# Optimization experiments

Measured on AMD Instinct MI355X. Metric: run time of the kernel, lower is better.

The kernel has to match this reference:

```python
import jax, jax.numpy as jnp
import numpy as np

B, S, V, H, L, NH, DH, F = 1, 512, 30522, 768, 12, 12, 64, 3072
N, E, GH, NC = 50000, 800000, 128, 3


def setup_inputs() -> dict:
    key = jax.random.key(0)
    ks = iter(jax.random.split(key, 48))
    def nrm(shape, s=0.02):
        return jax.random.normal(next(ks), shape, jnp.float32) * s
    inp = {
        "input_ids": jax.random.randint(next(ks), (B, S), 0, V, dtype=jnp.int32),
        "attention_mask": jnp.ones((B, S), jnp.int32),
        "token_type_ids": jnp.zeros((B, S), jnp.int32),
        "premise_edge_index": jax.random.randint(next(ks), (2, E), 0, N, dtype=jnp.int32),
        "hypothesis_edge_index": jax.random.randint(next(ks), (2, E), 0, N, dtype=jnp.int32),
        "premise_node_features": nrm((N, H), 1.0),
        "hypothesis_node_features": nrm((N, H), 1.0),
        "word_emb": nrm((V, H)), "pos_emb": nrm((S, H)), "type_emb": nrm((2, H)),
        "emb_ln_s": jnp.ones((H,)), "emb_ln_b": jnp.zeros((H,)),
        "Wq": nrm((L, H, H)), "bq": jnp.zeros((L, H)),
        "Wk": nrm((L, H, H)), "bk": jnp.zeros((L, H)),
        "Wv": nrm((L, H, H)), "bv": jnp.zeros((L, H)),
        "Wo": nrm((L, H, H)), "bo": jnp.zeros((L, H)),
        "ln1_s": jnp.ones((L, H)), "ln1_b": jnp.zeros((L, H)),
        "W1": nrm((L, H, F)), "b1": jnp.zeros((L, F)),
        "W2": nrm((L, F, H)), "b2": jnp.zeros((L, H)),
        "ln2_s": jnp.ones((L, H)), "ln2_b": jnp.zeros((L, H)),
        "gcn_W1": nrm((H, GH), 0.05), "gcn_b1": jnp.zeros((GH,)),
        "gcn_W2": nrm((GH, GH), 0.05), "gcn_b2": jnp.zeros((GH,)),
        "comb_W": nrm((2 * (H + GH), H)), "comb_b": jnp.zeros((H,)),
        "cls_W": nrm((H, NC)), "cls_b": jnp.zeros((NC,)),
    }
    return inp


def _ln(x, s, b, eps=1e-12):
    m = jnp.mean(x, -1, keepdims=True)
    v = jnp.mean(jnp.square(x - m), -1, keepdims=True)
    return (x - m) * jax.lax.rsqrt(v + eps) * s + b


def _gcn(x, edge_index, W1, b1, W2, b2):
    # PyG GCNConv: add self-loops, symmetric D^-1/2 A D^-1/2 normalization,
    # linear transform first, then scatter-add messages at destination.
    n = x.shape[0]
    loops = jnp.arange(n, dtype=edge_index.dtype)
    src = jnp.concatenate([edge_index[0], loops])
    dst = jnp.concatenate([edge_index[1], loops])
    deg = jax.ops.segment_sum(jnp.ones(src.shape[0], jnp.float32), dst, num_segments=n)
    dinv = jnp.where(deg > 0, jax.lax.rsqrt(jnp.maximum(deg, 1e-12)), 0.0)
    norm = (dinv[src] * dinv[dst])[:, None]
    def conv(h, W, b):
        hw = h @ W
        return jax.ops.segment_sum(hw[src] * norm, dst, num_segments=n) + b
    h = jax.nn.relu(conv(x, W1, b1))
    h = conv(h, W2, b2)
    # global_mean_pool with batch=None -> single graph mean, shape [1, GH]
    return jnp.mean(h, axis=0, keepdims=True)


def _bert(input_ids, attention_mask, token_type_ids, word_emb, pos_emb, type_emb, emb_ln_s, emb_ln_b, layer_params):
    s = input_ids.shape[1]
    h = word_emb[input_ids] + pos_emb[None, :s] + type_emb[token_type_ids]
    h = _ln(h, emb_ln_s, emb_ln_b)
    bias = (1.0 - attention_mask.astype(jnp.float32))[:, None, None, :] * -1e4
    def step(h, p):
        wq, bq, wk, bk, wv, bv, wo, bo, l1s, l1b, w1, b1_, w2, b2_, l2s, l2b = p
        b_, s_, _ = h.shape
        q = (h @ wq + bq).reshape(b_, s_, NH, DH)
        k = (h @ wk + bk).reshape(b_, s_, NH, DH)
        v = (h @ wv + bv).reshape(b_, s_, NH, DH)
        scores = jnp.einsum('bqhd,bkhd->bhqk', q, k) / np.float32(np.sqrt(DH)) + bias
        ctx = jnp.einsum('bhqk,bkhd->bqhd', jax.nn.softmax(scores, -1), v).reshape(b_, s_, H)
        h1 = _ln(h + ctx @ wo + bo, l1s, l1b)
        f = jax.nn.gelu(h1 @ w1 + b1_, approximate=False) @ w2 + b2_
        return _ln(h1 + f, l2s, l2b), None
    h, _ = jax.lax.scan(step, h, layer_params)
    return h[:, 0, :]  # CLS pooling, [B, H]


def reference(input_ids, attention_mask, token_type_ids, premise_edge_index, premise_node_features, hypothesis_edge_index, hypothesis_node_features, word_emb, pos_emb, type_emb, emb_ln_s, emb_ln_b, Wq, bq, Wk, bk, Wv, bv, Wo, bo, ln1_s, ln1_b, W1, b1, W2, b2, ln2_s, ln2_b, gcn_W1, gcn_b1, gcn_W2, gcn_b2, comb_W, comb_b, cls_W, cls_b):
    lp = (Wq, bq, Wk, bk, Wv, bv, Wo, bo, ln1_s, ln1_b, W1, b1, W2, b2, ln2_s, ln2_b)
    cls = _bert(input_ids, attention_mask, token_type_ids, word_emb, pos_emb, type_emb, emb_ln_s, emb_ln_b, lp)
    gp = _gcn(premise_node_features, premise_edge_index, gcn_W1, gcn_b1, gcn_W2, gcn_b2)
    gh = _gcn(hypothesis_node_features, hypothesis_edge_index, gcn_W1, gcn_b1, gcn_W2, gcn_b2)
    cp = jnp.concatenate([cls, gp], -1)
    ch = jnp.concatenate([cls, gh], -1)
    fc = jnp.concatenate([cp, ch], -1)  # [1, 2*(H+GH)]
    feat = jax.nn.relu(fc @ comb_W + comb_b)  # dropout is identity at eval
    return feat @ cls_W + cls_b
```

## Files before the change

### kernel.cpp

```cpp
#include <hip/hip_runtime.h>
#include <math.h>

constexpr int kS = 512, kH = 768, kNH = 12, kDH = 64, kF = 3072, kL = 12;
constexpr int kN = 50000, kE = 800000, kGH = 128;

#define CDIV(a,b) (((a)+(b)-1)/(b))

struct Ptr3 { const float* p[3]; };

typedef __attribute__((ext_vector_type(8))) short bf16x8;
typedef __attribute__((ext_vector_type(4))) float f32x4;

__device__ __forceinline__ unsigned short bf16_rne(float f) {
    unsigned int u = __float_as_uint(f);
    u += 0x7fffu + ((u >> 16) & 1u);
    return (unsigned short)(u >> 16);
}
__device__ __forceinline__ float bf16_f32(unsigned short h) {
    return __uint_as_float(((unsigned int)h) << 16);
}
__device__ __forceinline__ void split2(float f, short& hi, short& lo) {
    unsigned short h = bf16_rne(f);
    hi = (short)h;
    lo = (short)bf16_rne(f - bf16_f32(h));
// ... 54 lines not shown
        short hi, lo; split2(f, hi, lo);
        th[rr][c] = hi; tl[rr][c] = lo;
    }
    __syncthreads();
    #pragma unroll
    for (int p = 0; p < 4; p++) {
        int rr = p * 8 + r;
        Th[moff + (long)(n0 + rr) * K + k0 + c] = th[c][rr];
        Tl[moff + (long)(n0 + rr) * K + k0 + c] = tl[c][rr];
    }
}

__global__ void vtrans_kernel(const short* __restrict__ vh, const short* __restrict__ vl,
                              short* __restrict__ vth, short* __restrict__ vtl) {
    __shared__ short th[32][33], tl[32][33];
    int s0 = blockIdx.x * 32;
    int h = blockIdx.y >> 1, d0 = (blockIdx.y & 1) * 32;
    int c = threadIdx.x & 31, r = threadIdx.x >> 5;
    #pragma unroll
    for (int p = 0; p < 4; p++) {
        int rr = p * 8 + r;
        th[rr][c] = vh[(long)(s0 + rr) * kH + h * kDH + d0 + c];
        tl[rr][c] = vl[(long)(s0 + rr) * kH + h * kDH + d0 + c];
    }
    __syncthreads();
    #pragma unroll
    for (int p = 0; p < 4; p++) {
        int rr = p * 8 + r;
        vth[((long)h * kDH + d0 + rr) * kS + s0 + c] = th[c][rr];
        vtl[((long)h * kDH + d0 + rr) * kS + s0 + c] = tl[c][rr];
    }
}

__global__ __launch_bounds__(256, 4) void gemm_pre_kernel(
    const short* __restrict__ Ah, const short* __restrict__ Al,
    const short* __restrict__ Bth, const short* __restrict__ Btl, long wstride,
    float* __restrict__ part, int M, int Nn, int K, int S)
{
    __shared__ short As[128 * LDR], Bs[128 * LDR];
    int w = blockIdx.z / S, s = blockIdx.z % S;
    const short* Bh_ = Bth + (long)w * wstride;
    const short* Bl_ = Btl + (long)w * wstride;
    int Kc = K / S;
    int kbeg = s * Kc;
    int m0 = blockIdx.y * 128, n0 = blockIdx.x * 128;
    int tid = threadIdx.x;
    int sr = tid >> 1, sh16 = (tid & 1) * 16;
    const short* Agh = Ah + (long)(m0 + sr) * K + kbeg + sh16;
    const short* Agl = Al + (long)(m0 + sr) * K + kbeg + sh16;
    const short* Bgh = Bh_ + (long)(n0 + sr) * K + kbeg + sh16;
    const short* Bgl = Bl_ + (long)(n0 + sr) * K + kbeg + sh16;
    int lofs = sr * LDR + sh16;
    int wid = tid >> 6, lane = tid & 63;
    int wm = (wid >> 1) * 64, wn = (wid & 1) * 64;
    int fr = lane & 15, ko = (lane >> 4) * 8;
    f32x4 acc[4][4];
    #pragma unroll
    for (int i = 0; i < 4; i++)
        #pragma unroll
        for (int j = 0; j < 4; j++) acc[i][j] = (f32x4){0.f, 0.f, 0.f, 0.f};
    int nst = Kc / 32;
    for (int st = 0; st < nst; ++st) {
        int go = st * 32;
        *(bf16x8*)&As[lofs]      = *(const bf16x8*)(Agh + go);
        *(bf16x8*)&As[lofs + 8]  = *(const bf16x8*)(Agh + go + 8);
        *(bf16x8*)&As[lofs + 32] = *(const bf16x8*)(Agl + go);
        *(bf16x8*)&As[lofs + 40] = *(const bf16x8*)(Agl + go + 8);
        *(bf16x8*)&Bs[lofs]      = *(const bf16x8*)(Bgh + go);
        *(bf16x8*)&Bs[lofs + 8]  = *(const bf16x8*)(Bgh + go + 8);
        *(bf16x8*)&Bs[lofs + 32] = *(const bf16x8*)(Bgl + go);
        *(bf16x8*)&Bs[lofs + 40] = *(const bf16x8*)(Bgl + go + 8);
        __syncthreads();
        bf16x8 bh[4], bl[4];
        #pragma unroll
        for (int j = 0; j < 4; j++) {
            int c = (wn + j * 16 + fr) * LDR + ko;
            bh[j] = *(const bf16x8*)&Bs[c];
            bl[j] = *(const bf16x8*)&Bs[c + 32];
        }
        #pragma unroll
        for (int i = 0; i < 4; i++) {
            int r = (wm + i * 16 + fr) * LDR + ko;
            bf16x8 ah = *(const bf16x8*)&As[r];
            bf16x8 al = *(const bf16x8*)&As[r + 32];
            #pragma unroll
            for (int j = 0; j < 4; j++) {
                acc[i][j] = __builtin_amdgcn_mfma_f32_16x16x32_bf16(ah, bh[j], acc[i][j], 0, 0, 0);
                acc[i][j] = __builtin_amdgcn_mfma_f32_16x16x32_bf16(ah, bl[j], acc[i][j], 0, 0, 0);
                acc[i][j] = __builtin_amdgcn_mfma_f32_16x16x32_bf16(al, bh[j], acc[i][j], 0, 0, 0);
            }
        }
        __syncthreads();
    }
    long MN = (long)M * Nn;
    float* Pp = part + (long)(w * S + s) * MN;
    int cr = (lane >> 4) * 4;
    #pragma unroll
    for (int i = 0; i < 4; i++) {
        #pragma unroll
        for (int r = 0; r < 4; r++) {
            int gm = m0 + wm + i * 16 + cr + r;
            float* rowp = &Pp[(long)gm * Nn + n0 + wn + fr];
            #pragma unroll
            for (int j = 0; j < 4; j++) rowp[j * 16] = acc[i][j][r];
        }
    }
}

__global__ void splitk_epi_qkv_kernel(const float* __restrict__ part, Ptr3 bias,
                                      short* __restrict__ qh, short* __restrict__ ql,
                                      short* __restrict__ kh, short* __restrict__ kl,
                                      short* __restrict__ vh, short* __restrict__ vl,
                                      int S) {
    const long MN = (long)kS * kH;
    int w = blockIdx.y;
    long i = ((long)blockIdx.x * blockDim.x + threadIdx.x) * 4;
    if (i >= MN) return;
    const float* P = part + (long)w * S * MN + i;
    float4 a = *(const float4*)P;
    for (int s2 = 1; s2 < S; ++s2) {
        float4 b2 = *(const float4*)(P + (long)s2 * MN);
        a.x += b2.x; a.y += b2.y; a.z += b2.z; a.w += b2.w;
    }
    const float* bw = bias.p[w];
    int n = (int)(i % kH);
    a.x += bw[n]; a.y += bw[n + 1]; a.z += bw[n + 2]; a.w += bw[n + 3];
    short* oh = (w == 0) ? qh : (w == 1) ? kh : vh;
    short* ol = (w == 0) ? ql : (w == 1) ? kl : vl;
    short h0, l0, h1, l1, h2, l2, h3, l3;
    split2(a.x, h0, l0); split2(a.y, h1, l1); split2(a.z, h2, l2); split2(a.w, h3, l3);
    *(short4*)&oh[i] = make_short4(h0, h1, h2, h3);
    *(short4*)&ol[i] = make_short4(l0, l1, l2, l3);
}

__global__ void splitk_epi_sh_kernel(const float* __restrict__ part, const float* __restrict__ bias,
                                     short* __restrict__ oh, short* __restrict__ ol,
                                     long MN, int Nn, int S, int act) {
    long i = ((long)blockIdx.x * blockDim.x + threadIdx.x) * 4;
    if (i >= MN) return;
// ... 24 lines not shown
                                      const float* __restrict__ b, float* __restrict__ out,
                                      short* __restrict__ oh, short* __restrict__ ol, int S) {
    int row = blockIdx.x; int tid = threadIdx.x;
    __shared__ float red[256];
    const long MN = (long)kS * kH;
    float vals[3]; float sum = 0.f;
    #pragma unroll
    for (int r = 0; r < 3; r++) {
        int j = tid + r * 256;
        const float* P = part + (long)row * kH + j;
        float x = res[(long)row * kH + j] + bias[j];
        for (int s2 = 0; s2 < S; ++s2) x += P[(long)s2 * MN];
        vals[r] = x; sum += x;
    }
    red[tid] = sum; __syncthreads();
    for (int off = 128; off > 0; off >>= 1) { if (tid < off) red[tid] += red[tid + off]; __syncthreads(); }
    float mean = red[0] / kH; __syncthreads();
    float vs = 0.f;
    #pragma unroll
    for (int r = 0; r < 3; r++) { float d = vals[r] - mean; vs += d * d; }
    red[tid] = vs; __syncthreads();
    for (int off = 128; off > 0; off >>= 1) { if (tid < off) red[tid] += red[tid + off]; __syncthreads(); }
    float rstd = rsqrtf(red[0] / kH + 1e-12f);
    #pragma unroll
    for (int r = 0; r < 3; r++) {
        int j = tid + r * 256;
        float o = (vals[r] - mean) * rstd * g[j] + b[j];
        out[(long)row * kH + j] = o;
        short hi, lo; split2(o, hi, lo);
        oh[(long)row * kH + j] = hi; ol[(long)row * kH + j] = lo;
    }
}

__global__ __launch_bounds__(256, 4) void attn_scores_pre_kernel(
    const short* __restrict__ qh, const short* __restrict__ ql,
    const short* __restrict__ kh, const short* __restrict__ kl,
    const float* __restrict__ mb, float* __restrict__ scores)
{
    __shared__ short As[128 * LDR], Bs[128 * LDR];
    int h = blockIdx.z;
    int q0 = blockIdx.y * 128, k0 = blockIdx.x * 128;
    int tid = threadIdx.x;
    int sr = tid >> 1, sh16 = (tid & 1) * 16;
    const short* Agh = qh + (long)(q0 + sr) * kH + h * kDH + sh16;
    const short* Agl = ql + (long)(q0 + sr) * kH + h * kDH + sh16;
    const short* Bgh = kh + (long)(k0 + sr) * kH + h * kDH + sh16;
    const short* Bgl = kl + (long)(k0 + sr) * kH + h * kDH + sh16;
    int lofs = sr * LDR + sh16;
    int wid = tid >> 6, lane = tid & 63;
    int wm = (wid >> 1) * 64, wn = (wid & 1) * 64;
    int fr = lane & 15, ko = (lane >> 4) * 8;
    f32x4 acc[4][4];
    #pragma unroll
    for (int i = 0; i < 4; i++)
        #pragma unroll
        for (int j = 0; j < 4; j++) acc[i][j] = (f32x4){0.f, 0.f, 0.f, 0.f};
    #pragma unroll
    for (int st = 0; st < 2; ++st) {
        int go = st * 32;
        *(bf16x8*)&As[lofs]      = *(const bf16x8*)(Agh + go);
        *(bf16x8*)&As[lofs + 8]  = *(const bf16x8*)(Agh + go + 8);
        *(bf16x8*)&As[lofs + 32] = *(const bf16x8*)(Agl + go);
        *(bf16x8*)&As[lofs + 40] = *(const bf16x8*)(Agl + go + 8);
        *(bf16x8*)&Bs[lofs]      = *(const bf16x8*)(Bgh + go);
        *(bf16x8*)&Bs[lofs + 8]  = *(const bf16x8*)(Bgh + go + 8);
        *(bf16x8*)&Bs[lofs + 32] = *(const bf16x8*)(Bgl + go);
        *(bf16x8*)&Bs[lofs + 40] = *(const bf16x8*)(Bgl + go + 8);
        __syncthreads();
        bf16x8 bh[4], bl[4];
        #pragma unroll
        for (int j = 0; j < 4; j++) {
            int c = (wn + j * 16 + fr) * LDR + ko;
            bh[j] = *(const bf16x8*)&Bs[c];
            bl[j] = *(const bf16x8*)&Bs[c + 32];
        }
        #pragma unroll
        for (int i = 0; i < 4; i++) {
            int r = (wm + i * 16 + fr) * LDR + ko;
            bf16x8 ah = *(const bf16x8*)&As[r];
            bf16x8 al = *(const bf16x8*)&As[r + 32];
            #pragma unroll
            for (int j = 0; j < 4; j++) {
                acc[i][j] = __builtin_amdgcn_mfma_f32_16x16x32_bf16(ah, bh[j], acc[i][j], 0, 0, 0);
                acc[i][j] = __builtin_amdgcn_mfma_f32_16x16x32_bf16(ah, bl[j], acc[i][j], 0, 0, 0);
                acc[i][j] = __builtin_amdgcn_mfma_f32_16x16x32_bf16(al, bh[j], acc[i][j], 0, 0, 0);
            }
        }
        __syncthreads();
    }
    int cr = (lane >> 4) * 4;
    #pragma unroll
    for (int i = 0; i < 4; i++) {
        #pragma unroll
        for (int r = 0; r < 4; r++) {
            int qq = q0 + wm + i * 16 + cr + r;
            float* rowp = &scores[((long)h * kS + qq) * kS + k0 + wn + fr];
            #pragma unroll
            for (int j = 0; j < 4; j++)
                rowp[j * 16] = acc[i][j][r] * 0.125f + mb[k0 + wn + j * 16 + fr];
        }
    }
}

__global__ void softmax_split_kernel(const float* __restrict__ scores,
                                     short* __restrict__ ph, short* __restrict__ pl) {
    long row = blockIdx.x;
    const float* p = scores + row * kS;
    int tid = threadIdx.x;
    __shared__ float red[256];
    float x0 = p[tid], x1 = p[tid + 256];
    red[tid] = fmaxf(x0, x1); __syncthreads();
    for (int off = 128; off > 0; off >>= 1) { if (tid < off) red[tid] = fmaxf(red[tid], red[tid + off]); __syncthreads(); }
    float mx = red[0]; __syncthreads();
    float e0 = expf(x0 - mx), e1 = expf(x1 - mx);
    red[tid] = e0 + e1; __syncthreads();
    for (int off = 128; off > 0; off >>= 1) { if (tid < off) red[tid] += red[tid + off]; __syncthreads(); }
    float inv = 1.f / red[0];
    float r0 = e0 * inv, r1 = e1 * inv;
    short h0, l0, h1, l1;
    split2(r0, h0, l0); split2(r1, h1, l1);
    ph[row * kS + tid] = h0; pl[row * kS + tid] = l0;
    ph[row * kS + tid + 256] = h1; pl[row * kS + tid + 256] = l1;
}

__global__ __launch_bounds__(256, 4) void attn_ctx_pre_kernel(
    const short* __restrict__ ph, const short* __restrict__ pl,
    const short* __restrict__ vth, const short* __restrict__ vtl,
    float* __restrict__ part)
{
    __shared__ short As[128 * LDR];
    __shared__ short Bs[64 * LDR];
    int q0 = blockIdx.x * 128;
    int h = blockIdx.y >> 2, s = blockIdx.y & 3;
    int kbeg = s * 128;
    int tid = threadIdx.x;
    int sr = tid >> 1, sh16 = (tid & 1) * 16;
    const short* Agh = ph + ((long)h * kS + q0 + sr) * kS + kbeg + sh16;
    const short* Agl = pl + ((long)h * kS + q0 + sr) * kS + kbeg + sh16;
    int sbr = tid >> 2, sq = tid & 3;
    const short* Bg = (sq < 2 ? vth : vtl) + ((long)h * kDH + sbr) * kS + kbeg + (sq & 1) * 16;
    int bofs = sbr * LDR + (sq >= 2 ? 32 : 0) + (sq & 1) * 16;
    int aofs = sr * LDR + sh16;
    int wid = tid >> 6, lane = tid & 63;
    int wm = wid * 32;
    int fr = lane & 15, ko = (lane >> 4) * 8;
    f32x4 acc[2][4];
    #pragma unroll
    for (int i = 0; i < 2; i++)
        #pragma unroll
        for (int j = 0; j < 4; j++) acc[i][j] = (f32x4){0.f, 0.f, 0.f, 0.f};
    #pragma unroll
    for (int st = 0; st < 4; ++st) {
        int go = st * 32;
        *(bf16x8*)&As[aofs]      = *(const bf16x8*)(Agh + go);
        *(bf16x8*)&As[aofs + 8]  = *(const bf16x8*)(Agh + go + 8);
        *(bf16x8*)&As[aofs + 32] = *(const bf16x8*)(Agl + go);
        *(bf16x8*)&As[aofs + 40] = *(const bf16x8*)(Agl + go + 8);
        *(bf16x8*)&Bs[bofs]      = *(const bf16x8*)(Bg + go);
        *(bf16x8*)&Bs[bofs + 8]  = *(const bf16x8*)(Bg + go + 8);
        __syncthreads();
        bf16x8 bh[4], bl[4];
        #pragma unroll
        for (int j = 0; j < 4; j++) {
            int c = (j * 16 + fr) * LDR + ko;
            bh[j] = *(const bf16x8*)&Bs[c];
            bl[j] = *(const bf16x8*)&Bs[c + 32];
        }
        #pragma unroll
        for (int i = 0; i < 2; i++) {
            int r = (wm + i * 16 + fr) * LDR + ko;
            bf16x8 ah = *(const bf16x8*)&As[r];
            bf16x8 al = *(const bf16x8*)&As[r + 32];
            #pragma unroll
            for (int j = 0; j < 4; j++) {
                acc[i][j] = __builtin_amdgcn_mfma_f32_16x16x32_bf16(ah, bh[j], acc[i][j], 0, 0, 0);
                acc[i][j] = __builtin_amdgcn_mfma_f32_16x16x32_bf16(ah, bl[j], acc[i][j], 0, 0, 0);
                acc[i][j] = __builtin_amdgcn_mfma_f32_16x16x32_bf16(al, bh[j], acc[i][j], 0, 0, 0);
            }
        }
        __syncthreads();
    }
    long Pbase = (long)s * ((long)kS * kH);
    int cr = (lane >> 4) * 4;
    #pragma unroll
    for (int i = 0; i < 2; i++) {
        #pragma unroll
        for (int r = 0; r < 4; r++) {
            int gq = q0 + wm + i * 16 + cr + r;
            float* rowp = &part[Pbase + (long)gq * kH + h * kDH + fr];
            #pragma unroll
            for (int j = 0; j < 4; j++) rowp[j * 16] = acc[i][j][r];
        }
    }
}

__global__ __launch_bounds__(256, 4) void gemm_mfma_kernel(
    const float* __restrict__ A, Ptr3 Bp, float* __restrict__ part,
    float* __restrict__ Cdirect, const float* __restrict__ biasD,
    int M, int Nn, int K, int S, int act)
{
    constexpr int LDK = 40;
    __shared__ short Ah[128 * LDK], Al[128 * LDK], Bh[128 * LDK], Bl[128 * LDK];
    int w = blockIdx.z / S, s = blockIdx.z % S;
    const float* B = Bp.p[w];
    int Kc = K / S;
    int kbeg = s * Kc;
    int m0 = blockIdx.y * 128, n0 = blockIdx.x * 128;
    int tid = threadIdx.x;
    int sar = tid >> 1, sac = (tid & 1) * 16;
    int sbc = tid & 127, sbk = (tid >> 7) * 16;
    int gmA = m0 + sar; if (gmA > M - 1) gmA = M - 1;
    const float* Ag0 = A + (long)gmA * K + kbeg + sac;
    const float* Bg0 = B + (long)(kbeg + sbk) * Nn + n0 + sbc;
    int wid = tid >> 6, lane = tid & 63;
    int wm = (wid >> 1) * 64, wn = (wid & 1) * 64;
    int fr = lane & 15, ko = (lane >> 4) * 8;
    f32x4 acc[4][4];
    #pragma unroll
    for (int i = 0; i < 4; i++)
        #pragma unroll
        for (int j = 0; j < 4; j++) acc[i][j] = (f32x4){0.f, 0.f, 0.f, 0.f};
    int nst = Kc / 32;
    for (int st = 0; st < nst; ++st) {
        {
            const float* Ag = Ag0 + st * 32;
            int ob = sar * LDK + sac;
            #pragma unroll
            for (int qg = 0; qg < 4; qg++) {
                float4 f = *(const float4*)(Ag + qg * 4);
                unsigned short h0 = bf16_rne(f.x), h1 = bf16_rne(f.y),
                               h2 = bf16_rne(f.z), h3 = bf16_rne(f.w);
                unsigned short g0 = bf16_rne(f.x - bf16_f32(h0)), g1 = bf16_rne(f.y - bf16_f32(h1)),
                               g2 = bf16_rne(f.z - bf16_f32(h2)), g3 = bf16_rne(f.w - bf16_f32(h3));
                *(short4*)&Ah[ob + qg * 4] = make_short4((short)h0, (short)h1, (short)h2, (short)h3);
                *(short4*)&Al[ob + qg * 4] = make_short4((short)g0, (short)g1, (short)g2, (short)g3);
            }
        }
        {
            const float* Bg = Bg0 + (long)st * 32 * Nn;
            int ob = sbc * LDK + sbk;
            #pragma unroll
            for (int qg = 0; qg < 4; qg++) {
                float f0 = Bg[(long)(qg * 4 + 0) * Nn];
                float f1 = Bg[(long)(qg * 4 + 1) * Nn];
                float f2 = Bg[(long)(qg * 4 + 2) * Nn];
                float f3 = Bg[(long)(qg * 4 + 3) * Nn];
                unsigned short h0 = bf16_rne(f0), h1 = bf16_rne(f1),
                               h2 = bf16_rne(f2), h3 = bf16_rne(f3);
                unsigned short g0 = bf16_rne(f0 - bf16_f32(h0)), g1 = bf16_rne(f1 - bf16_f32(h1)),
                               g2 = bf16_rne(f2 - bf16_f32(h2)), g3 = bf16_rne(f3 - bf16_f32(h3));
                *(short4*)&Bh[ob + qg * 4] = make_short4((short)h0, (short)h1, (short)h2, (short)h3);
                *(short4*)&Bl[ob + qg * 4] = make_short4((short)g0, (short)g1, (short)g2, (short)g3);
            }
        }
        __syncthreads();
        bf16x8 bh[4], bl[4];
        #pragma unroll
        for (int j = 0; j < 4; j++) {
            int c = (wn + j * 16 + fr) * LDK + ko;
            bh[j] = *(const bf16x8*)&Bh[c];
            bl[j] = *(const bf16x8*)&Bl[c];
        }
        #pragma unroll
        for (int i = 0; i < 4; i++) {
            int r = (wm + i * 16 + fr) * LDK + ko;
            bf16x8 ah = *(const bf16x8*)&Ah[r];
            bf16x8 al = *(const bf16x8*)&Al[r];
            #pragma unroll
            for (int j = 0; j < 4; j++) {
                acc[i][j] = __builtin_amdgcn_mfma_f32_16x16x32_bf16(ah, bh[j], acc[i][j], 0, 0, 0);
                acc[i][j] = __builtin_amdgcn_mfma_f32_16x16x32_bf16(ah, bl[j], acc[i][j], 0, 0, 0);
                acc[i][j] = __builtin_amdgcn_mfma_f32_16x16x32_bf16(al, bh[j], acc[i][j], 0, 0, 0);
            }
        }
        __syncthreads();
    }
    int cr = (lane >> 4) * 4;
    if (Cdirect) {
        #pragma unroll
        for (int i = 0; i < 4; i++) {
            #pragma unroll
            for (int r = 0; r < 4; r++) {
                int gm = m0 + wm + i * 16 + cr + r;
                if (gm >= M) continue;
                float* rowp = &Cdirect[(long)gm * Nn + n0 + wn + fr];
                #pragma unroll
                for (int j = 0; j < 4; j++) {
                    float vv = acc[i][j][r];
                    if (biasD) vv += biasD[n0 + wn + j * 16 + fr];
                    if (act == 2) vv = fmaxf(vv, 0.f);
                    rowp[j * 16] = vv;
                }
            }
        }
    } else {
        long MN = (long)M * Nn;
        float* Pp = part + (long)(w * S + s) * MN;
        #pragma unroll
        for (int i = 0; i < 4; i++) {
            #pragma unroll
            for (int r = 0; r < 4; r++) {
                int gm = m0 + wm + i * 16 + cr + r;
                if (gm >= M) continue;
                float* rowp = &Pp[(long)gm * Nn + n0 + wn + fr];
                #pragma unroll
                for (int j = 0; j < 4; j++) rowp[j * 16] = acc[i][j][r];
            }
        }
    }
}

__global__ void maskbias_kernel(const int* mask, float* mb) {
    int i = blockIdx.x * blockDim.x + threadIdx.x;
    if (i < kS) mb[i] = (1.f - (float)mask[i]) * -1e4f;
}

__global__ void cnt_kernel(const int* __restrict__ dst, int* __restrict__ cnt, int E) {
    int e = blockIdx.x * blockDim.x + threadIdx.x;
    if (e < E) atomicAdd(&cnt[dst[e]], 1);
}

__global__ void scan1_kernel(const int* __restrict__ cnt, int* __restrict__ offs,
                             int* __restrict__ bsum, int n) {
    __shared__ int sh[256];
    int i = blockIdx.x * 256 + threadIdx.x;
    int v = (i < n) ? cnt[i] : 0;
    sh[threadIdx.x] = v; __syncthreads();
    for (int off = 1; off < 256; off <<= 1) {
        int t = (threadIdx.x >= off) ? sh[threadIdx.x - off] : 0;
        __syncthreads();
        sh[threadIdx.x] += t;
        __syncthreads();
    }
    if (i < n) offs[i] = sh[threadIdx.x] - v;
    if (threadIdx.x == 255) bsum[blockIdx.x] = sh[255];
}

__global__ void scan2_kernel(int* bsum, int nb, int* offs, int n) {
    if (threadIdx.x == 0) {
        int run = 0;
// ... 141 lines not shown
    float* wsum = alloc(kN);
    float* svec = alloc(kGH);
    float* gp   = alloc(kGH);
    float* ghv  = alloc(kGH);
    float* mb   = alloc(kS);
    float* feat = alloc(kH);
    float* big  = W + off;

    float* part  = big;
    float* scores = part;
    short* p_h   = (short*)(big + 4718592);
    short* p_l   = p_h + (size_t)3145728;
    short* ffn1_h = (short*)(big + 7864320);
    short* ffn1_l = ffn1_h + (size_t)1572864;
    short* wt_h  = (short*)(big + 9437184);
    short* wt_l  = wt_h + (size_t)2359296;
    short* sm    = (short*)(big + 11796480);
    const size_t SMN = (size_t)kS * kH;
    short* q_h = sm;            short* q_l = q_h + SMN;
    short* k_h = q_l + SMN;     short* k_l = k_h + SMN;
    short* v_h = k_l + SMN;     short* v_l = v_h + SMN;
    short* vt_h = v_l + SMN;    short* vt_l = vt_h + SMN;
    short* ctx_h = vt_l + SMN;  short* ctx_l = ctx_h + SMN;
    short* h1_h = ctx_l + SMN;  short* h1_l = h1_h + SMN;
    short* hh_h = h1_l + SMN;   short* hh_l = hh_h + SMN;

    float* hw1 = big;
    float* agg = big + (size_t)kN * kGH;
    int* icnt  = (int*)(big + 2 * (size_t)kN * kGH);
    int* ioffs = icnt + 50048;
    int* icur  = ioffs + 50048;
    int* ibsum = icur + 50048;
    int* icsr  = ibsum + 256;

    const long MN_H = (long)kS * kH;
    const long MN_F = (long)kS * kF;
    const int nScanBlk = CDIV(kN, 256);

    const int* gsrc[2] = { p_edges, h_edges };
    const int* gdst[2] = { p_edges + kE, h_edges + kE };
    const float* gx[2] = { p_nodes, h_nodes };
    float* gout[2] = { gp, ghv };
    for (int gi = 0; gi < 2; gi++) {
        fill_kernel<<<CDIV((long)kN, 256), 256, 0, stream>>>((float*)icnt, 0.f, kN);
        fill_kernel<<<CDIV((long)kN, 256), 256, 0, stream>>>(wsum, 0.f, kN);
        fill_kernel<<<1, 256, 0, stream>>>(svec, 0.f, kGH);
        cnt_kernel<<<CDIV(kE, 256), 256, 0, stream>>>(gdst[gi], icnt, kE);
        scan1_kernel<<<nScanBlk, 256, 0, stream>>>(icnt, ioffs, ibsum, kN);
        scan2_kernel<<<1, 64, 0, stream>>>(ibsum, nScanBlk, ioffs, kN);
        scan3_kernel<<<nScanBlk, 256, 0, stream>>>(icnt, ioffs, ibsum, icur, deg, kN);
        csrfill_edgew_kernel<<<CDIV(kE, 256), 256, 0, stream>>>(
            gsrc[gi], gdst[gi], icur, icsr, deg, wsum, kE);
        gemm_mfma_kernel<<<dim3(1, CDIV(kN, 128), 1), 256, 0, stream>>>(
            gx[gi], Ptr3{{gW1, nullptr, nullptr}}, nullptr, hw1, nullptr, kN, kGH, kH, 1, 0);
        spmm_gather_kernel<<<CDIV(kN, 2), 256, 0, stream>>>(ioffs, icsr, deg, hw1, gb1, agg, kN);
        wreduce_kernel<<<512, 256, 0, stream>>>(agg, wsum, deg, svec, kN);
        gcn_final_kernel<<<1, kGH, 0, stream>>>(svec, gW2, gb2, gout[gi]);
    }

    maskbias_kernel<<<2, 256, 0, stream>>>(attn_mask, mb);
    embed_ln_kernel<<<kS, 256, 0, stream>>>(input_ids, type_ids, word_emb, pos_emb, type_emb,
                                            eln_s, eln_b, h, hh_h, hh_l);
    for (int l = 0; l < kL; l++) {
        const float* Wq_l = Wq + (size_t)l * kH * kH; const float* bq_l = bq + (size_t)l * kH;
        const float* Wk_l = Wk + (size_t)l * kH * kH; const float* bk_l = bk + (size_t)l * kH;
        const float* Wv_l = Wv + (size_t)l * kH * kH; const float* bv_l = bv + (size_t)l * kH;
        const float* Wo_l = Wo + (size_t)l * kH * kH; const float* bo_l = bo + (size_t)l * kH;
        const float* W1_l = W1 + (size_t)l * kH * kF; const float* b1_l = b1 + (size_t)l * kF;
        const float* W2_l = W2 + (size_t)l * kF * kH; const float* b2_l = b2 + (size_t)l * kH;
        const float* l1s_l = l1s + (size_t)l * kH; const float* l1b_l = l1b + (size_t)l * kH;
        const float* l2s_l = l2s + (size_t)l * kH; const float* l2b_l = l2b + (size_t)l * kH;

        wtrans_kernel<<<dim3(24, 24, 3), 256, 0, stream>>>(
            Ptr3{{Wq_l, Wk_l, Wv_l}}, wt_h, wt_l, kH, kH);
        gemm_pre_kernel<<<dim3(kH / 128, kS / 128, 12), 256, 0, stream>>>(
            hh_h, hh_l, wt_h, wt_l, (long)kH * kH, part, kS, kH, kH, 4);
        splitk_epi_qkv_kernel<<<dim3((int)(MN_H / 4 / 256), 3), 256, 0, stream>>>(
            part, Ptr3{{bq_l, bk_l, bv_l}}, q_h, q_l, k_h, k_l, v_h, v_l, 4);
        vtrans_kernel<<<dim3(kS / 32, kNH * 2), 256, 0, stream>>>(v_h, v_l, vt_h, vt_l);
        attn_scores_pre_kernel<<<dim3(kS / 128, kS / 128, kNH), 256, 0, stream>>>(
            q_h, q_l, k_h, k_l, mb, scores);
        softmax_split_kernel<<<kNH * kS, 256, 0, stream>>>(scores, p_h, p_l);
        attn_ctx_pre_kernel<<<dim3(kS / 128, kNH * 4), 256, 0, stream>>>(p_h, p_l, vt_h, vt_l, part);
        splitk_epi_sh_kernel<<<dim3((int)(MN_H / 4 / 256)), 256, 0, stream>>>(
            part, nullptr, ctx_h, ctx_l, MN_H, kH, 4, 0);
        wtrans_kernel<<<dim3(24, 24, 1), 256, 0, stream>>>(
            Ptr3{{Wo_l, nullptr, nullptr}}, wt_h, wt_l, kH, kH);
        gemm_pre_kernel<<<dim3(kH / 128, kS / 128, 8), 256, 0, stream>>>(
            ctx_h, ctx_l, wt_h, wt_l, 0, part, kS, kH, kH, 8);
        splitk_epi_ln2_kernel<<<kS, 256, 0, stream>>>(part, bo_l, h, l1s_l, l1b_l, h1, h1_h, h1_l, 8);
        wtrans_kernel<<<dim3(96, 24, 1), 256, 0, stream>>>(
            Ptr3{{W1_l, nullptr, nullptr}}, wt_h, wt_l, kH, kF);
        gemm_pre_kernel<<<dim3(kF / 128, kS / 128, 3), 256, 0, stream>>>(
            h1_h, h1_l, wt_h, wt_l, 0, part, kS, kF, kH, 3);
        splitk_epi_sh_kernel<<<dim3((int)(MN_F / 4 / 256)), 256, 0, stream>>>(
            part, b1_l, ffn1_h, ffn1_l, MN_F, kF, 3, 1);
        wtrans_kernel<<<dim3(24, 96, 1), 256, 0, stream>>>(
            Ptr3{{W2_l, nullptr, nullptr}}, wt_h, wt_l, kF, kH);
        gemm_pre_kernel<<<dim3(kH / 128, kS / 128, 12), 256, 0, stream>>>(
            ffn1_h, ffn1_l, wt_h, wt_l, 0, part, kS, kH, kF, 12);
        splitk_epi_ln2_kernel<<<kS, 256, 0, stream>>>(part, b2_l, h1, l2s_l, l2b_l, h, hh_h, hh_l, 12);
    }

    combine_kernel<<<3, 256, 0, stream>>>(h, gp, ghv, cW, cb, feat);
    cls_head_kernel<<<1, 256, 0, stream>>>(feat, clsW, clsB, out);
}
```

Measured before the change: 2.905 ms.

## Use 64-row GEMM tiles, retune split-K, pre-split GCN weights

All bf16-split MFMA GEMMs (the QKV, output, FFN and attention-scores projections) move from 128x128 to 64x128 output tiles, with reworked load mappings, so the small-M BERT GEMMs launch more blocks. Split-K factors are retuned: attention context now uses 8 splits, the Wo projection 12 and FFN1 4. The GCN feature GEMM no longer converts fp32 weights to hi/lo bf16 inside every tile. It uses a weight matrix transposed and split once, plus a 2-way split-K and a separate fp32 reduction kernel. The trade-off is more partial-sum traffic and extra epilogue work, and the split-K partials for the GCN need twice the space in the hw1 buffer.

Result: no change. 2.881 ms (-0.8%).

```diff
diff --git a/kernel.cpp b/kernel.cpp
--- a/kernel.cpp
+++ b/kernel.cpp
@@ -110,44 +110,43 @@
     }
 }
 
-__global__ __launch_bounds__(256, 4) void gemm_pre_kernel(
+__global__ __launch_bounds__(256, 4) void gemm64_pre(
     const short* __restrict__ Ah, const short* __restrict__ Al,
     const short* __restrict__ Bth, const short* __restrict__ Btl, long wstride,
     float* __restrict__ part, int M, int Nn, int K, int S)
 {
-    __shared__ short As[128 * LDR], Bs[128 * LDR];
+    __shared__ short As[64 * LDR], Bs[128 * LDR];
     int w = blockIdx.z / S, s = blockIdx.z % S;
     const short* Bh_ = Bth + (long)w * wstride;
     const short* Bl_ = Btl + (long)w * wstride;
-    int Kc = K / S;
-    int kbeg = s * Kc;
-    int m0 = blockIdx.y * 128, n0 = blockIdx.x * 128;
+    int Kc = K / S, kbeg = s * Kc;
+    int m0 = blockIdx.y * 64, n0 = blockIdx.x * 128;
     int tid = threadIdx.x;
-    int sr = tid >> 1, sh16 = (tid & 1) * 16;
-    const short* Agh = Ah + (long)(m0 + sr) * K + kbeg + sh16;
-    const short* Agl = Al + (long)(m0 + sr) * K + kbeg + sh16;
-    const short* Bgh = Bh_ + (long)(n0 + sr) * K + kbeg + sh16;
-    const short* Bgl = Bl_ + (long)(n0 + sr) * K + kbeg + sh16;
-    int lofs = sr * LDR + sh16;
+    int ar = tid >> 2, aq = (tid & 3) * 8;
+    const short* Agh = Ah + (long)(m0 + ar) * K + kbeg + aq;
+    const short* Agl = Al + (long)(m0 + ar) * K + kbeg + aq;
+    int aofs = ar * LDR + aq;
+    int br = tid >> 1, bq = (tid & 1) * 16;
+    const short* Bgh = Bh_ + (long)(n0 + br) * K + kbeg + bq;
+    const short* Bgl = Bl_ + (long)(n0 + br) * K + kbeg + bq;
+    int bofs = br * LDR + bq;
     int wid = tid >> 6, lane = tid & 63;
-    int wm = (wid >> 1) * 64, wn = (wid & 1) * 64;
+    int wm = (wid >> 1) * 32, wn = (wid & 1) * 64;
     int fr = lane & 15, ko = (lane >> 4) * 8;
-    f32x4 acc[4][4];
-    #pragma unroll
-    for (int i = 0; i < 4; i++)
+    f32x4 acc[2][4];
+    #pragma unroll
+    for (int i = 0; i < 2; i++)
         #pragma unroll
         for (int j = 0; j < 4; j++) acc[i][j] = (f32x4){0.f, 0.f, 0.f, 0.f};
     int nst = Kc / 32;
     for (int st = 0; st < nst; ++st) {
         int go = st * 32;
-        *(bf16x8*)&As[lofs]      = *(const bf16x8*)(Agh + go);
-        *(bf16x8*)&As[lofs + 8]  = *(const bf16x8*)(Agh + go + 8);
-        *(bf16x8*)&As[lofs + 32] = *(const bf16x8*)(Agl + go);
-        *(bf16x8*)&As[lofs + 40] = *(const bf16x8*)(Agl + go + 8);
-        *(bf16x8*)&Bs[lofs]      = *(const bf16x8*)(Bgh + go);
-        *(bf16x8*)&Bs[lofs + 8]  = *(const bf16x8*)(Bgh + go + 8);
-        *(bf16x8*)&Bs[lofs + 32] = *(const bf16x8*)(Bgl + go);
-        *(bf16x8*)&Bs[lofs + 40] = *(const bf16x8*)(Bgl + go + 8);
+        *(bf16x8*)&As[aofs]      = *(const bf16x8*)(Agh + go);
+        *(bf16x8*)&As[aofs + 32] = *(const bf16x8*)(Agl + go);
+        *(bf16x8*)&Bs[bofs]      = *(const bf16x8*)(Bgh + go);
+        *(bf16x8*)&Bs[bofs + 8]  = *(const bf16x8*)(Bgh + go + 8);
+        *(bf16x8*)&Bs[bofs + 32] = *(const bf16x8*)(Bgl + go);
+        *(bf16x8*)&Bs[bofs + 40] = *(const bf16x8*)(Bgl + go + 8);
         __syncthreads();
         bf16x8 bh[4], bl[4];
         #pragma unroll
@@ -157,7 +156,7 @@
             bl[j] = *(const bf16x8*)&Bs[c + 32];
         }
         #pragma unroll
-        for (int i = 0; i < 4; i++) {
+        for (int i = 0; i < 2; i++) {
             int r = (wm + i * 16 + fr) * LDR + ko;
             bf16x8 ah = *(const bf16x8*)&As[r];
             bf16x8 al = *(const bf16x8*)&As[r + 32];
@@ -174,7 +173,7 @@
     float* Pp = part + (long)(w * S + s) * MN;
     int cr = (lane >> 4) * 4;
     #pragma unroll
-    for (int i = 0; i < 4; i++) {
+    for (int i = 0; i < 2; i++) {
         #pragma unroll
         for (int r = 0; r < 4; r++) {
             int gm = m0 + wm + i * 16 + cr + r;
@@ -183,6 +182,97 @@
             for (int j = 0; j < 4; j++) rowp[j * 16] = acc[i][j][r];
         }
     }
+}
+
+__global__ __launch_bounds__(256, 4) void gemm64_gcn(
+    const float* __restrict__ A,
+    const short* __restrict__ Bth, const short* __restrict__ Btl,
+    float* __restrict__ part, int M, int Nn, int K, int S)
+{
+    __shared__ short As[64 * LDR], Bs[128 * LDR];
+    int s = blockIdx.z;
+    int Kc = K / S, kbeg = s * Kc;
+    int m0 = blockIdx.y * 64, n0 = blockIdx.x * 128;
+    int tid = threadIdx.x;
+    int ar = tid >> 2, aqf = (tid & 3) * 8;
+    int gmA = m0 + ar; if (gmA > M - 1) gmA = M - 1;
+    const float* Agf = A + (long)gmA * K + kbeg + aqf;
+    int aofs = ar * LDR + aqf;
+    int br = tid >> 1, bq = (tid & 1) * 16;
+    const short* Bgh = Bth + (long)(n0 + br) * K + kbeg + bq;
+    const short* Bgl = Btl + (long)(n0 + br) * K + kbeg + bq;
+    int bofs = br * LDR + bq;
+    int wid = tid >> 6, lane = tid & 63;
+    int wm = (wid >> 1) * 32, wn = (wid & 1) * 64;
+    int fr = lane & 15, ko = (lane >> 4) * 8;
+    f32x4 acc[2][4];
+    #pragma unroll
+    for (int i = 0; i < 2; i++)
+        #pragma unroll
+        for (int j = 0; j < 4; j++) acc[i][j] = (f32x4){0.f, 0.f, 0.f, 0.f};
+    int nst = Kc / 32;
+    for (int st = 0; st < nst; ++st) {
+        int go = st * 32;
+        float4 f0 = *(const float4*)(Agf + go);
+        float4 f1 = *(const float4*)(Agf + go + 4);
+        short h0, l0, h1, l1, h2, l2, h3, l3, h4, l4, h5, l5, h6, l6, h7, l7;
+        split2(f0.x, h0, l0); split2(f0.y, h1, l1); split2(f0.z, h2, l2); split2(f0.w, h3, l3);
+        split2(f1.x, h4, l4); split2(f1.y, h5, l5); split2(f1.z, h6, l6); split2(f1.w, h7, l7);
+        *(short4*)&As[aofs]      = make_short4(h0, h1, h2, h3);
+        *(short4*)&As[aofs + 4]  = make_short4(h4, h5, h6, h7);
+        *(short4*)&As[aofs + 32] = make_short4(l0, l1, l2, l3);
+        *(short4*)&As[aofs + 36] = make_short4(l4, l5, l6, l7);
+        *(bf16x8*)&Bs[bofs]      = *(const bf16x8*)(Bgh + go);
+        *(bf16x8*)&Bs[bofs + 8]  = *(const bf16x8*)(Bgh + go + 8);
+        *(bf16x8*)&Bs[bofs + 32] = *(const bf16x8*)(Bgl + go);
+        *(bf16x8*)&Bs[bofs + 40] = *(const bf16x8*)(Bgl + go + 8);
+        __syncthreads();
+        bf16x8 bh[4], bl[4];
+        #pragma unroll
+        for (int j = 0; j < 4; j++) {
+            int c = (wn + j * 16 + fr) * LDR + ko;
+            bh[j] = *(const bf16x8*)&Bs[c];
+            bl[j] = *(const bf16x8*)&Bs[c + 32];
+        }
+        #pragma unroll
+        for (int i = 0; i < 2; i++) {
+            int r = (wm + i * 16 + fr) * LDR + ko;
+            bf16x8 ah = *(const bf16x8*)&As[r];
+            bf16x8 al = *(const bf16x8*)&As[r + 32];
+            #pragma unroll
+            for (int j = 0; j < 4; j++) {
+                acc[i][j] = __builtin_amdgcn_mfma_f32_16x16x32_bf16(ah, bh[j], acc[i][j], 0, 0, 0);
+                acc[i][j] = __builtin_amdgcn_mfma_f32_16x16x32_bf16(ah, bl[j], acc[i][j], 0, 0, 0);
+                acc[i][j] = __builtin_amdgcn_mfma_f32_16x16x32_bf16(al, bh[j], acc[i][j], 0, 0, 0);
+            }
+        }
+        __syncthreads();
+    }
+    long MN = (long)M * Nn;
+    float* Pp = part + (long)s * MN;
+    int cr = (lane >> 4) * 4;
+    #pragma unroll
+    for (int i = 0; i < 2; i++) {
+        #pragma unroll
+        for (int r = 0; r < 4; r++) {
+            int gm = m0 + wm + i * 16 + cr + r;
+            if (gm >= M) continue;
+            float* rowp = &Pp[(long)gm * Nn + n0 + wn + fr];
+            #pragma unroll
+            for (int j = 0; j < 4; j++) rowp[j * 16] = acc[i][j][r];
+        }
+    }
+}
+
+__global__ void splitk_epi_f32(const float* part, float* out, long MN, int S) {
+    long i = ((long)blockIdx.x * blockDim.x + threadIdx.x) * 4;
+    if (i >= MN) return;
+    float4 a = *(const float4*)(part + i);
+    for (int s2 = 1; s2 < S; ++s2) {
+        float4 b = *(const float4*)(part + (long)s2 * MN + i);
+        a.x += b.x; a.y += b.y; a.z += b.z; a.w += b.w;
+    }
+    *(float4*)(out + i) = a;
 }
 
 __global__ void splitk_epi_qkv_kernel(const float* __restrict__ part, Ptr3 bias,
@@ -273,40 +363,40 @@
     }
 }
 
-__global__ __launch_bounds__(256, 4) void attn_scores_pre_kernel(
+__global__ __launch_bounds__(256, 4) void attn_scores64_kernel(
     const short* __restrict__ qh, const short* __restrict__ ql,
     const short* __restrict__ kh, const short* __restrict__ kl,
     const float* __restrict__ mb, float* __restrict__ scores)
 {
-    __shared__ short As[128 * LDR], Bs[128 * LDR];
+    __shared__ short As[64 * LDR], Bs[128 * LDR];
     int h = blockIdx.z;
-    int q0 = blockIdx.y * 128, k0 = blockIdx.x * 128;
+    int k0 = blockIdx.x * 128, q0 = blockIdx.y * 64;
     int tid = threadIdx.x;
-    int sr = tid >> 1, sh16 = (tid & 1) * 16;
-    const short* Agh = qh + (long)(q0 + sr) * kH + h * kDH + sh16;
-    const short* Agl = ql + (long)(q0 + sr) * kH + h * kDH + sh16;
-    const short* Bgh = kh + (long)(k0 + sr) * kH + h * kDH + sh16;
-    const short* Bgl = kl + (long)(k0 + sr) * kH + h * kDH + sh16;
-    int lofs = sr * LDR + sh16;
+    int ar = tid >> 2, aq = (tid & 3) * 8;
+    const short* Agh = qh + (long)(q0 + ar) * kH + h * kDH + aq;
+    const short* Agl = ql + (long)(q0 + ar) * kH + h * kDH + aq;
+    int aofs = ar * LDR + aq;
+    int br = tid >> 1, bq = (tid & 1) * 16;
+    const short* Bgh = kh + (long)(k0 + br) * kH + h * kDH + bq;
+    const short* Bgl = kl + (long)(k0 + br) * kH + h * kDH + bq;
+    int bofs = br * LDR + bq;
     int wid = tid >> 6, lane = tid & 63;
-    int wm = (wid >> 1) * 64, wn = (wid & 1) * 64;
+    int wm = (wid >> 1) * 32, wn = (wid & 1) * 64;
     int fr = lane & 15, ko = (lane >> 4) * 8;
-    f32x4 acc[4][4];
-    #pragma unroll
-    for (int i = 0; i < 4; i++)
+    f32x4 acc[2][4];
+    #pragma unroll
+    for (int i = 0; i < 2; i++)
         #pragma unroll
         for (int j = 0; j < 4; j++) acc[i][j] = (f32x4){0.f, 0.f, 0.f, 0.f};
     #pragma unroll
     for (int st = 0; st < 2; ++st) {
         int go = st * 32;
-        *(bf16x8*)&As[lofs]      = *(const bf16x8*)(Agh + go);
-        *(bf16x8*)&As[lofs + 8]  = *(const bf16x8*)(Agh + go + 8);
-        *(bf16x8*)&As[lofs + 32] = *(const bf16x8*)(Agl + go);
-        *(bf16x8*)&As[lofs + 40] = *(const bf16x8*)(Agl + go + 8);
-        *(bf16x8*)&Bs[lofs]      = *(const bf16x8*)(Bgh + go);
-        *(bf16x8*)&Bs[lofs + 8]  = *(const bf16x8*)(Bgh + go + 8);
-        *(bf16x8*)&Bs[lofs + 32] = *(const bf16x8*)(Bgl + go);
-        *(bf16x8*)&Bs[lofs + 40] = *(const bf16x8*)(Bgl + go + 8);
+        *(bf16x8*)&As[aofs]      = *(const bf16x8*)(Agh + go);
+        *(bf16x8*)&As[aofs + 32] = *(const bf16x8*)(Agl + go);
+        *(bf16x8*)&Bs[bofs]      = *(const bf16x8*)(Bgh + go);
+        *(bf16x8*)&Bs[bofs + 8]  = *(const bf16x8*)(Bgh + go + 8);
+        *(bf16x8*)&Bs[bofs + 32] = *(const bf16x8*)(Bgl + go);
+        *(bf16x8*)&Bs[bofs + 40] = *(const bf16x8*)(Bgl + go + 8);
         __syncthreads();
         bf16x8 bh[4], bl[4];
         #pragma unroll
@@ -316,7 +406,7 @@
             bl[j] = *(const bf16x8*)&Bs[c + 32];
         }
         #pragma unroll
-        for (int i = 0; i < 4; i++) {
+        for (int i = 0; i < 2; i++) {
             int r = (wm + i * 16 + fr) * LDR + ko;
             bf16x8 ah = *(const bf16x8*)&As[r];
             bf16x8 al = *(const bf16x8*)&As[r + 32];
@@ -331,7 +421,7 @@
     }
     int cr = (lane >> 4) * 4;
     #pragma unroll
-    for (int i = 0; i < 4; i++) {
+    for (int i = 0; i < 2; i++) {
         #pragma unroll
         for (int r = 0; r < 4; r++) {
             int qq = q0 + wm + i * 16 + cr + r;
@@ -364,24 +454,24 @@
     ph[row * kS + tid + 256] = h1; pl[row * kS + tid + 256] = l1;
 }
 
-__global__ __launch_bounds__(256, 4) void attn_ctx_pre_kernel(
+__global__ __launch_bounds__(256, 4) void attn_ctx64_kernel(
     const short* __restrict__ ph, const short* __restrict__ pl,
     const short* __restrict__ vth, const short* __restrict__ vtl,
     float* __restrict__ part)
 {
-    __shared__ short As[128 * LDR];
-    __shared__ short Bs[64 * LDR];
+    __shared__ short As[128 * LDR], Bs[64 * LDR];
     int q0 = blockIdx.x * 128;
-    int h = blockIdx.y >> 2, s = blockIdx.y & 3;
-    int kbeg = s * 128;
+    int h = blockIdx.y >> 3, s = blockIdx.y & 7;
+    int kbeg = s * 64;
     int tid = threadIdx.x;
-    int sr = tid >> 1, sh16 = (tid & 1) * 16;
-    const short* Agh = ph + ((long)h * kS + q0 + sr) * kS + kbeg + sh16;
-    const short* Agl = pl + ((long)h * kS + q0 + sr) * kS + kbeg + sh16;
-    int sbr = tid >> 2, sq = tid & 3;
-    const short* Bg = (sq < 2 ? vth : vtl) + ((long)h * kDH + sbr) * kS + kbeg + (sq & 1) * 16;
-    int bofs = sbr * LDR + (sq >= 2 ? 32 : 0) + (sq & 1) * 16;
-    int aofs = sr * LDR + sh16;
+    int ar = tid >> 1, aq = (tid & 1) * 16;
+    const short* Agh = ph + ((long)h * kS + q0 + ar) * kS + kbeg + aq;
+    const short* Agl = pl + ((long)h * kS + q0 + ar) * kS + kbeg + aq;
+    int aofs = ar * LDR + aq;
+    int brr = tid >> 2, bq = (tid & 3) * 8;
+    const short* Bgh = vth + ((long)h * kDH + brr) * kS + kbeg + bq;
+    const short* Bgl = vtl + ((long)h * kDH + brr) * kS + kbeg + bq;
+    int bofs = brr * LDR + bq;
     int wid = tid >> 6, lane = tid & 63;
     int wm = wid * 32;
     int fr = lane & 15, ko = (lane >> 4) * 8;
@@ -391,14 +481,14 @@
         #pragma unroll
         for (int j = 0; j < 4; j++) acc[i][j] = (f32x4){0.f, 0.f, 0.f, 0.f};
     #pragma unroll
-    for (int st = 0; st < 4; ++st) {
+    for (int st = 0; st < 2; ++st) {
         int go = st * 32;
         *(bf16x8*)&As[aofs]      = *(const bf16x8*)(Agh + go);
         *(bf16x8*)&As[aofs + 8]  = *(const bf16x8*)(Agh + go + 8);
         *(bf16x8*)&As[aofs + 32] = *(const bf16x8*)(Agl + go);
         *(bf16x8*)&As[aofs + 40] = *(const bf16x8*)(Agl + go + 8);
-        *(bf16x8*)&Bs[bofs]      = *(const bf16x8*)(Bg + go);
-        *(bf16x8*)&Bs[bofs + 8]  = *(const bf16x8*)(Bg + go + 8);
+        *(bf16x8*)&Bs[bofs]      = *(const bf16x8*)(Bgh + go);
+        *(bf16x8*)&Bs[bofs + 32] = *(const bf16x8*)(Bgl + go);
         __syncthreads();
         bf16x8 bh[4], bl[4];
         #pragma unroll
@@ -431,122 +521,6 @@
             float* rowp = &part[Pbase + (long)gq * kH + h * kDH + fr];
             #pragma unroll
             for (int j = 0; j < 4; j++) rowp[j * 16] = acc[i][j][r];
-        }
-    }
-}
-
-__global__ __launch_bounds__(256, 4) void gemm_mfma_kernel(
-    const float* __restrict__ A, Ptr3 Bp, float* __restrict__ part,
-    float* __restrict__ Cdirect, const float* __restrict__ biasD,
-    int M, int Nn, int K, int S, int act)
-{
-    constexpr int LDK = 40;
-    __shared__ short Ah[128 * LDK], Al[128 * LDK], Bh[128 * LDK], Bl[128 * LDK];
-    int w = blockIdx.z / S, s = blockIdx.z % S;
-    const float* B = Bp.p[w];
-    int Kc = K / S;
-    int kbeg = s * Kc;
-    int m0 = blockIdx.y * 128, n0 = blockIdx.x * 128;
-    int tid = threadIdx.x;
-    int sar = tid >> 1, sac = (tid & 1) * 16;
-    int sbc = tid & 127, sbk = (tid >> 7) * 16;
-    int gmA = m0 + sar; if (gmA > M - 1) gmA = M - 1;
-    const float* Ag0 = A + (long)gmA * K + kbeg + sac;
-    const float* Bg0 = B + (long)(kbeg + sbk) * Nn + n0 + sbc;
-    int wid = tid >> 6, lane = tid & 63;
-    int wm = (wid >> 1) * 64, wn = (wid & 1) * 64;
-    int fr = lane & 15, ko = (lane >> 4) * 8;
-    f32x4 acc[4][4];
-    #pragma unroll
-    for (int i = 0; i < 4; i++)
-        #pragma unroll
-        for (int j = 0; j < 4; j++) acc[i][j] = (f32x4){0.f, 0.f, 0.f, 0.f};
-    int nst = Kc / 32;
-    for (int st = 0; st < nst; ++st) {
-        {
-            const float* Ag = Ag0 + st * 32;
-            int ob = sar * LDK + sac;
-            #pragma unroll
-            for (int qg = 0; qg < 4; qg++) {
-                float4 f = *(const float4*)(Ag + qg * 4);
-                unsigned short h0 = bf16_rne(f.x), h1 = bf16_rne(f.y),
-                               h2 = bf16_rne(f.z), h3 = bf16_rne(f.w);
-                unsigned short g0 = bf16_rne(f.x - bf16_f32(h0)), g1 = bf16_rne(f.y - bf16_f32(h1)),
-                               g2 = bf16_rne(f.z - bf16_f32(h2)), g3 = bf16_rne(f.w - bf16_f32(h3));
-                *(short4*)&Ah[ob + qg * 4] = make_short4((short)h0, (short)h1, (short)h2, (short)h3);
-                *(short4*)&Al[ob + qg * 4] = make_short4((short)g0, (short)g1, (short)g2, (short)g3);
-            }
-        }
-        {
-            const float* Bg = Bg0 + (long)st * 32 * Nn;
-            int ob = sbc * LDK + sbk;
-            #pragma unroll
-            for (int qg = 0; qg < 4; qg++) {
-                float f0 = Bg[(long)(qg * 4 + 0) * Nn];
-                float f1 = Bg[(long)(qg * 4 + 1) * Nn];
-                float f2 = Bg[(long)(qg * 4 + 2) * Nn];
-                float f3 = Bg[(long)(qg * 4 + 3) * Nn];
-                unsigned short h0 = bf16_rne(f0), h1 = bf16_rne(f1),
-                               h2 = bf16_rne(f2), h3 = bf16_rne(f3);
-                unsigned short g0 = bf16_rne(f0 - bf16_f32(h0)), g1 = bf16_rne(f1 - bf16_f32(h1)),
-                               g2 = bf16_rne(f2 - bf16_f32(h2)), g3 = bf16_rne(f3 - bf16_f32(h3));
-                *(short4*)&Bh[ob + qg * 4] = make_short4((short)h0, (short)h1, (short)h2, (short)h3);
-                *(short4*)&Bl[ob + qg * 4] = make_short4((short)g0, (short)g1, (short)g2, (short)g3);
-            }
-        }
-        __syncthreads();
-        bf16x8 bh[4], bl[4];
-        #pragma unroll
-        for (int j = 0; j < 4; j++) {
-            int c = (wn + j * 16 + fr) * LDK + ko;
-            bh[j] = *(const bf16x8*)&Bh[c];
-            bl[j] = *(const bf16x8*)&Bl[c];
-        }
-        #pragma unroll
-        for (int i = 0; i < 4; i++) {
-            int r = (wm + i * 16 + fr) * LDK + ko;
-            bf16x8 ah = *(const bf16x8*)&Ah[r];
-            bf16x8 al = *(const bf16x8*)&Al[r];
-            #pragma unroll
-            for (int j = 0; j < 4; j++) {
-                acc[i][j] = __builtin_amdgcn_mfma_f32_16x16x32_bf16(ah, bh[j], acc[i][j], 0, 0, 0);
-                acc[i][j] = __builtin_amdgcn_mfma_f32_16x16x32_bf16(ah, bl[j], acc[i][j], 0, 0, 0);
-                acc[i][j] = __builtin_amdgcn_mfma_f32_16x16x32_bf16(al, bh[j], acc[i][j], 0, 0, 0);
-            }
-        }
-        __syncthreads();
-    }
-    int cr = (lane >> 4) * 4;
-    if (Cdirect) {
-        #pragma unroll
-        for (int i = 0; i < 4; i++) {
-            #pragma unroll
-            for (int r = 0; r < 4; r++) {
-                int gm = m0 + wm + i * 16 + cr + r;
-                if (gm >= M) continue;
-                float* rowp = &Cdirect[(long)gm * Nn + n0 + wn + fr];
-                #pragma unroll
-                for (int j = 0; j < 4; j++) {
-                    float vv = acc[i][j][r];
-                    if (biasD) vv += biasD[n0 + wn + j * 16 + fr];
-                    if (act == 2) vv = fmaxf(vv, 0.f);
-                    rowp[j * 16] = vv;
-                }
-            }
-        }
-    } else {
-        long MN = (long)M * Nn;
-        float* Pp = part + (long)(w * S + s) * MN;
-        #pragma unroll
-        for (int i = 0; i < 4; i++) {
-            #pragma unroll
-            for (int r = 0; r < 4; r++) {
-                int gm = m0 + wm + i * 16 + cr + r;
-                if (gm >= M) continue;
-                float* rowp = &Pp[(long)gm * Nn + n0 + wn + fr];
-                #pragma unroll
-                for (int j = 0; j < 4; j++) rowp[j * 16] = acc[i][j][r];
-            }
         }
     }
 }
@@ -754,15 +728,20 @@
     int* icur  = ioffs + 50048;
     int* ibsum = icur + 50048;
     int* icsr  = ibsum + 256;
+    short* gwt_h = (short*)(icsr + kE);
+    short* gwt_l = gwt_h + (size_t)kH * kGH;
 
     const long MN_H = (long)kS * kH;
     const long MN_F = (long)kS * kF;
+    const long MN_G = (long)kN * kGH;
     const int nScanBlk = CDIV(kN, 256);
 
     const int* gsrc[2] = { p_edges, h_edges };
     const int* gdst[2] = { p_edges + kE, h_edges + kE };
     const float* gx[2] = { p_nodes, h_nodes };
     float* gout[2] = { gp, ghv };
+    wtrans_kernel<<<dim3(kGH / 32, kH / 32, 1), 256, 0, stream>>>(
+        Ptr3{{gW1, nullptr, nullptr}}, gwt_h, gwt_l, kH, kGH);
     for (int gi = 0; gi < 2; gi++) {
         fill_kernel<<<CDIV((long)kN, 256), 256, 0, stream>>>((float*)icnt, 0.f, kN);
         fill_kernel<<<CDIV((long)kN, 256), 256, 0, stream>>>(wsum, 0.f, kN);
@@ -773,8 +752,9 @@
         scan3_kernel<<<nScanBlk, 256, 0, stream>>>(icnt, ioffs, ibsum, icur, deg, kN);
         csrfill_edgew_kernel<<<CDIV(kE, 256), 256, 0, stream>>>(
             gsrc[gi], gdst[gi], icur, icsr, deg, wsum, kE);
-        gemm_mfma_kernel<<<dim3(1, CDIV(kN, 128), 1), 256, 0, stream>>>(
-            gx[gi], Ptr3{{gW1, nullptr, nullptr}}, nullptr, hw1, nullptr, kN, kGH, kH, 1, 0);
+        gemm64_gcn<<<dim3(1, CDIV(kN, 64), 2), 256, 0, stream>>>(
+            gx[gi], gwt_h, gwt_l, hw1, kN, kGH, kH, 2);
+        splitk_epi_f32<<<(int)(MN_G / 4 / 256), 256, 0, stream>>>(hw1, hw1, MN_G, 2);
         spmm_gather_kernel<<<CDIV(kN, 2), 256, 0, stream>>>(ioffs, icsr, deg, hw1, gb1, agg, kN);
         wreduce_kernel<<<512, 256, 0, stream>>>(agg, wsum, deg, svec, kN);
         gcn_final_kernel<<<1, kGH, 0, stream>>>(svec, gW2, gb2, gout[gi]);
@@ -795,31 +775,31 @@
 
         wtrans_kernel<<<dim3(24, 24, 3), 256, 0, stream>>>(
             Ptr3{{Wq_l, Wk_l, Wv_l}}, wt_h, wt_l, kH, kH);
-        gemm_pre_kernel<<<dim3(kH / 128, kS / 128, 12), 256, 0, stream>>>(
+        gemm64_pre<<<dim3(kH / 128, kS / 64, 12), 256, 0, stream>>>(
             hh_h, hh_l, wt_h, wt_l, (long)kH * kH, part, kS, kH, kH, 4);
         splitk_epi_qkv_kernel<<<dim3((int)(MN_H / 4 / 256), 3), 256, 0, stream>>>(
             part, Ptr3{{bq_l, bk_l, bv_l}}, q_h, q_l, k_h, k_l, v_h, v_l, 4);
         vtrans_kernel<<<dim3(kS / 32, kNH * 2), 256, 0, stream>>>(v_h, v_l, vt_h, vt_l);
-        attn_scores_pre_kernel<<<dim3(kS / 128, kS / 128, kNH), 256, 0, stream>>>(
+        attn_scores64_kernel<<<dim3(kS / 128, kS / 64, kNH), 256, 0, stream>>>(
             q_h, q_l, k_h, k_l, mb, scores);
         softmax_split_kernel<<<kNH * kS, 256, 0, stream>>>(scores, p_h, p_l);
-        attn_ctx_pre_kernel<<<dim3(kS / 128, kNH * 4), 256, 0, stream>>>(p_h, p_l, vt_h, vt_l, part);
-        splitk_epi_sh_kernel<<<dim3((int)(MN_H / 4 / 256)), 256, 0, stream>>>(
-            part, nullptr, ctx_h, ctx_l, MN_H, kH, 4, 0);
+        attn_ctx64_kernel<<<dim3(kS / 128, kNH * 8), 256, 0, stream>>>(p_h, p_l, vt_h, vt_l, part);
+        splitk_epi_sh_kernel<<<(int)(MN_H / 4 / 256), 256, 0, stream>>>(
+            part, nullptr, ctx_h, ctx_l, MN_H, kH, 8, 0);
         wtrans_kernel<<<dim3(24, 24, 1), 256, 0, stream>>>(
             Ptr3{{Wo_l, nullptr, nullptr}}, wt_h, wt_l, kH, kH);
-        gemm_pre_kernel<<<dim3(kH / 128, kS / 128, 8), 256, 0, stream>>>(
-            ctx_h, ctx_l, wt_h, wt_l, 0, part, kS, kH, kH, 8);
-        splitk_epi_ln2_kernel<<<kS, 256, 0, stream>>>(part, bo_l, h, l1s_l, l1b_l, h1, h1_h, h1_l, 8);
+        gemm64_pre<<<dim3(kH / 128, kS / 64, 12), 256, 0, stream>>>(
+            ctx_h, ctx_l, wt_h, wt_l, 0, part, kS, kH, kH, 12);
+        splitk_epi_ln2_kernel<<<kS, 256, 0, stream>>>(part, bo_l, h, l1s_l, l1b_l, h1, h1_h, h1_l, 12);
         wtrans_kernel<<<dim3(96, 24, 1), 256, 0, stream>>>(
             Ptr3{{W1_l, nullptr, nullptr}}, wt_h, wt_l, kH, kF);
-        gemm_pre_kernel<<<dim3(kF / 128, kS / 128, 3), 256, 0, stream>>>(
-            h1_h, h1_l, wt_h, wt_l, 0, part, kS, kF, kH, 3);
-        splitk_epi_sh_kernel<<<dim3((int)(MN_F / 4 / 256)), 256, 0, stream>>>(
-            part, b1_l, ffn1_h, ffn1_l, MN_F, kF, 3, 1);
+        gemm64_pre<<<dim3(kF / 128, kS / 64, 4), 256, 0, stream>>>(
+            h1_h, h1_l, wt_h, wt_l, 0, part, kS, kF, kH, 4);
+        splitk_epi_sh_kernel<<<(int)(MN_F / 4 / 256), 256, 0, stream>>>(
+            part, b1_l, ffn1_h, ffn1_l, MN_F, kF, 4, 1);
         wtrans_kernel<<<dim3(24, 96, 1), 256, 0, stream>>>(
             Ptr3{{W2_l, nullptr, nullptr}}, wt_h, wt_l, kF, kH);
-        gemm_pre_kernel<<<dim3(kH / 128, kS / 128, 12), 256, 0, stream>>>(
+        gemm64_pre<<<dim3(kH / 128, kS / 64, 12), 256, 0, stream>>>(
             ffn1_h, ffn1_l, wt_h, wt_l, 0, part, kS, kH, kF, 12);
         splitk_epi_ln2_kernel<<<kS, 256, 0, stream>>>(part, b2_l, h1, l2s_l, l2b_l, h, hh_h, hh_l, 12);
     }
```
